# Kernel tuning notes

Hardware: AMD Instinct MI355X
Metric: run time of the kernel (lower is better)

Reference implementation:

```python
import jax, jax.numpy as jnp
import numpy as np
from jax import lax

NODATA_VALUE = 0.0
RADIUS = 16  # structuring element size = 2*RADIUS + 1 = 33


def setup_inputs() -> dict:
    key = jax.random.key(0)
    # binary-ish raster: ~half pixels equal the nodata value (0.0)
    x = jax.random.randint(key, (8, 2048, 2048, 1), 0, 2).astype(jnp.float32)
    return {"x": x}


def reference(x):
    # nodata mask: 1 where x == nodata, else 0 (uint8 in original; float here for reduce_window)
    mask = jnp.where(jnp.equal(x, NODATA_VALUE), 1.0, 0.0).astype(x.dtype)
    se = 1 + 2 * RADIUS
    # tf.nn.dilation2d with an all-zeros kernel == sliding-window max over (se x se),
    # SAME padding. A square max window is separable: row-max then column-max.
    m = lax.reduce_window(mask, -jnp.inf, lax.max,
                          window_dimensions=(1, se, 1, 1),
                          window_strides=(1, 1, 1, 1),
                          padding="SAME")
    m = lax.reduce_window(m, -jnp.inf, lax.max,
                          window_dimensions=(1, 1, se, 1),
                          window_strides=(1, 1, 1, 1),
                          padding="SAME")
    return m.astype(jnp.uint8)
```

## Files before the change

kernel.cpp:

```cpp
#include <hip/hip_runtime.h>
#include <stdint.h>


#define NIMG 8
#define HH_ 2048
#define WW_PX 2048
#define WW 32
#define RAD 16

__device__ __forceinline__ uint64_t spread4(uint64_t x) {
  x &= 0xFFFFULL;
  x = (x | (x << 24)) & 0x000000FF000000FFULL;
  x = (x | (x << 12)) & 0x000F000F000F000FULL;
  x = (x | (x << 6))  & 0x0303030303030303ULL;
  x = (x | (x << 3))  & 0x1111111111111111ULL;
  return x;
}

__global__ __launch_bounds__(256) void pack_kernel(const float* __restrict__ x,
                                                   uint64_t* __restrict__ packed) {
  const long long px0 = ((long long)blockIdx.x * 256 + threadIdx.x) * 4;
  const float4 v = *(const float4*)(x + px0);
  const unsigned long long m0 = __ballot(v.x == 0.0f);
  const unsigned long long m1 = __ballot(v.y == 0.0f);
  const unsigned long long m2 = __ballot(v.z == 0.0f);
  const unsigned long long m3 = __ballot(v.w == 0.0f);
  const int lane = threadIdx.x & 63;
  if ((lane & 15) == 0) {
    const int sh = lane;
    uint64_t w = spread4(m0 >> sh)
               | (spread4(m1 >> sh) << 1)
               | (spread4(m2 >> sh) << 2)
               | (spread4(m3 >> sh) << 3);
    packed[px0 >> 6] = w;
  }
}

__global__ __launch_bounds__(256) void dilate_kernel(const uint64_t* __restrict__ packed,
                                                     int* __restrict__ out) {
  __shared__ uint64_t vall[8][WW + 2];
  __shared__ uint64_t hrow[8][WW];

  const int t = threadIdx.x;
  const int w = t & 31;
  const int r = t >> 5;
  const int gr0 = blockIdx.x * 8;
  const int n = gr0 >> 11;
  const int h = (gr0 & 2047) + r;
  const uint64_t* base = packed + (long long)n * (HH_ * WW);

  uint64_t v = 0;
#pragma unroll
  for (int dh = -RAD; dh <= RAD; ++dh) {
    int hh = h + dh;
    hh = hh < 0 ? 0 : (hh > HH_ - 1 ? HH_ - 1 : hh);
    v |= base[hh * WW + w];
  }
  vall[r][w + 1] = v;
  if (w == 0) { vall[r][0] = 0; vall[r][WW + 1] = 0; }
  __syncthreads();

  {
    const uint64_t p = vall[r][w];
    const uint64_t c = vall[r][w + 1];
    const uint64_t nx = vall[r][w + 2];
    uint64_t res = c;
#pragma unroll
    for (int s = 1; s <= RAD; ++s) {
      res |= (c >> s) | (nx << (64 - s));
      res |= (c << s) | (p >> (64 - s));
    }
    hrow[r][w] = res;
  }
  __syncthreads();

  int* obase = out + (long long)gr0 * WW_PX;
#pragma unroll
  for (int it = 0; it < 16; ++it) {
    const int f = it * 256 + t;
    const int row_l = f >> 9;
    const int wi = (f >> 4) & 31;
    const int sh = (f & 15) * 4;
    const uint64_t bits = hrow[row_l][wi] >> sh;
    int4 o;
    o.x = (int)(bits & 1);
    o.y = (int)((bits >> 1) & 1);
    o.z = (int)((bits >> 2) & 1);
    o.w = (int)((bits >> 3) & 1);
    *(int4*)(obase + (long long)f * 4) = o;
  }
}

extern "C" void kernel_launch(void* const* d_in, const int* in_sizes, int n_in,
                              void* d_out, int out_size, void* d_ws, size_t ws_size,
                              hipStream_t stream) {
  const float* x = (const float*)d_in[0];
  int* out = (int*)d_out;
  uint64_t* packed = (uint64_t*)d_ws;

  hipLaunchKernelGGL(pack_kernel, dim3(32768), dim3(256), 0, stream, x, packed);
  hipLaunchKernelGGL(dilate_kernel, dim3(2048), dim3(256), 0, stream, packed, out);
}
```

Before: 229.9 us.

## Stage packed rows in LDS, double rows per block, use nontemporal loads/stores

```diff
diff --git a/kernel.cpp b/kernel.cpp
--- a/kernel.cpp
+++ b/kernel.cpp
@@ -2,11 +2,15 @@
 #include <stdint.h>
 
 
-#define NIMG 8
 #define HH_ 2048
 #define WW_PX 2048
 #define WW 32
 #define RAD 16
+#define ROWS 16
+#define TPB2 512
+
+typedef float  vfloat4 __attribute__((ext_vector_type(4)));
+typedef int    vint4   __attribute__((ext_vector_type(4)));
 
 __device__ __forceinline__ uint64_t spread4(uint64_t x) {
   x &= 0xFFFFULL;
@@ -20,7 +24,7 @@
 __global__ __launch_bounds__(256) void pack_kernel(const float* __restrict__ x,
                                                    uint64_t* __restrict__ packed) {
   const long long px0 = ((long long)blockIdx.x * 256 + threadIdx.x) * 4;
-  const float4 v = *(const float4*)(x + px0);
+  const vfloat4 v = __builtin_nontemporal_load((const vfloat4*)(x + px0));
   const unsigned long long m0 = __ballot(v.x == 0.0f);
   const unsigned long long m1 = __ballot(v.y == 0.0f);
   const unsigned long long m2 = __ballot(v.z == 0.0f);
@@ -36,26 +40,34 @@
   }
 }
 
-__global__ __launch_bounds__(256) void dilate_kernel(const uint64_t* __restrict__ packed,
-                                                     int* __restrict__ out) {
-  __shared__ uint64_t vall[8][WW + 2];
-  __shared__ uint64_t hrow[8][WW];
+__global__ __launch_bounds__(TPB2) void dilate_kernel(const uint64_t* __restrict__ packed,
+                                                      int* __restrict__ out) {
+  __shared__ uint64_t stage[ROWS + 2 * RAD][WW];
+  __shared__ uint64_t vall[ROWS][WW + 2];
+  __shared__ uint64_t hrow[ROWS][WW];
 
   const int t = threadIdx.x;
+  const int gr0 = blockIdx.x * ROWS;
+  const int n = gr0 >> 11;
+  const int h0 = gr0 & 2047;
+  const uint64_t* base = packed + (long long)n * (HH_ * WW);
+
+#pragma unroll
+  for (int i = 0; i < (ROWS + 2 * RAD) * WW / TPB2; ++i) {
+    const int idx = i * TPB2 + t;
+    const int rr = idx >> 5;
+    const int w_ = idx & 31;
+    int hh = h0 + rr - RAD;
+    hh = hh < 0 ? 0 : (hh > HH_ - 1 ? HH_ - 1 : hh);
+    stage[rr][w_] = base[hh * WW + w_];
+  }
+  __syncthreads();
+
   const int w = t & 31;
   const int r = t >> 5;
-  const int gr0 = blockIdx.x * 8;
-  const int n = gr0 >> 11;
-  const int h = (gr0 & 2047) + r;
-  const uint64_t* base = packed + (long long)n * (HH_ * WW);
-
   uint64_t v = 0;
 #pragma unroll
-  for (int dh = -RAD; dh <= RAD; ++dh) {
-    int hh = h + dh;
-    hh = hh < 0 ? 0 : (hh > HH_ - 1 ? HH_ - 1 : hh);
-    v |= base[hh * WW + w];
-  }
+  for (int i = 0; i <= 2 * RAD; ++i) v |= stage[r + i][w];
   vall[r][w + 1] = v;
   if (w == 0) { vall[r][0] = 0; vall[r][WW + 1] = 0; }
   __syncthreads();
@@ -77,17 +89,17 @@
   int* obase = out + (long long)gr0 * WW_PX;
 #pragma unroll
   for (int it = 0; it < 16; ++it) {
-    const int f = it * 256 + t;
+    const int f = it * TPB2 + t;
     const int row_l = f >> 9;
     const int wi = (f >> 4) & 31;
     const int sh = (f & 15) * 4;
     const uint64_t bits = hrow[row_l][wi] >> sh;
-    int4 o;
+    vint4 o;
     o.x = (int)(bits & 1);
     o.y = (int)((bits >> 1) & 1);
     o.z = (int)((bits >> 2) & 1);
     o.w = (int)((bits >> 3) & 1);
-    *(int4*)(obase + (long long)f * 4) = o;
+    __builtin_nontemporal_store(o, (vint4*)(obase + (long long)f * 4));
   }
 }
 
@@ -99,5 +111,5 @@
   uint64_t* packed = (uint64_t*)d_ws;
 
   hipLaunchKernelGGL(pack_kernel, dim3(32768), dim3(256), 0, stream, x, packed);
-  hipLaunchKernelGGL(dilate_kernel, dim3(2048), dim3(256), 0, stream, packed, out);
+  hipLaunchKernelGGL(dilate_kernel, dim3(1024), dim3(TPB2), 0, stream, packed, out);
 }
```

Measured after the change: 225.4 us. -2.0%, faster.
